# Kernel tuning notes

Measured on AMD Instinct MI355X. Metric: run time of the kernel, lower is better.

## Reference

```python
import jax, jax.numpy as jnp
import numpy as np

R = 32  # voxel resolution


def _swish(x):
    return x * jax.nn.sigmoid(x)


def _group_norm(x, gamma, beta, groups, eps=1e-5):
    B, C = x.shape[0], x.shape[1]
    xr = x.reshape(B, groups, -1)
    mean = xr.mean(-1, keepdims=True)
    var = xr.var(-1, keepdims=True)
    xn = ((xr - mean) * jax.lax.rsqrt(var + eps)).reshape(x.shape)
    bshape = (1, C) + (1,) * (x.ndim - 2)
    return xn * gamma.reshape(bshape) + beta.reshape(bshape)


def _conv3d_same(x, w, b):
    # x: [B,C,D,H,W], w: [O,I,k,k,k], SAME padding (k//2)
    k = w.shape[-1]
    p = k // 2
    y = jax.lax.conv_general_dilated(
        x, w, window_strides=(1, 1, 1), padding=[(p, p)] * 3,
        dimension_numbers=('NCDHW', 'OIDHW', 'NCDHW'))
    return y + b[None, :, None, None, None]


def setup_inputs() -> dict:
    key = jax.random.key(0)
    ks = jax.random.split(key, 8)
    B, Cin, Cout, N = 8, 64, 128, 16384
    return {
        'features': jax.random.normal(ks[0], (B, Cin, N), jnp.float32),
        'coords': jax.random.normal(ks[1], (B, 3, N), jnp.float32),
        'temb': jnp.zeros((1,), jnp.float32),
        'w1': jax.random.normal(ks[2], (Cout, Cin, 3, 3, 3), jnp.float32) * 0.02,
        'b1': jnp.zeros((Cout,), jnp.float32),
        'g1_gamma': jnp.ones((Cout,), jnp.float32),
        'g1_beta': jnp.zeros((Cout,), jnp.float32),
        'w2': jax.random.normal(ks[3], (Cout, Cout, 3, 3, 3), jnp.float32) * 0.02,
        'b2': jnp.zeros((Cout,), jnp.float32),
        'g2_gamma': jnp.ones((Cout,), jnp.float32),
        'g2_beta': jnp.zeros((Cout,), jnp.float32),
        'wp': jax.random.normal(ks[4], (Cout, Cin), jnp.float32) * 0.02,
        'bp': jnp.zeros((Cout,), jnp.float32),
        'gp_gamma': jnp.ones((Cout,), jnp.float32),
        'gp_beta': jnp.zeros((Cout,), jnp.float32),
    }


def reference(features, coords, temb, w1, b1, g1_gamma, g1_beta,
              w2, b2, g2_gamma, g2_beta, wp, bp, gp_gamma, gp_beta):
    B, Cin, N = features.shape
    Cout = w1.shape[0]

    # ---- Voxelization (coords are detached in original; no coord grads) ----
    coords_c = jax.lax.stop_gradient(coords)
    nc = coords_c - coords_c.mean(axis=2, keepdims=True)            # [B,3,N]
    nrm = jnp.linalg.norm(nc, axis=1, keepdims=True)                # [B,1,N]
    nc = nc / (nrm.max(axis=2, keepdims=True) * 2.0) + 0.5          # eps=0
    nc = jnp.clip(nc * R, 0.0, R - 1)                               # norm_coords
    vox_idx = jnp.clip(jnp.round(nc).astype(jnp.int32), 0, R - 1)   # [B,3,N]

    flat = (vox_idx[:, 0] * R + vox_idx[:, 1]) * R + vox_idx[:, 2]  # [B,N]
    seg = (flat + jnp.arange(B, dtype=flat.dtype)[:, None] * (R ** 3)).reshape(-1)
    feat_bn = features.transpose(0, 2, 1).reshape(B * N, Cin)       # [B*N,Cin]
    sums = jax.ops.segment_sum(feat_bn, seg, num_segments=B * R ** 3)
    cnts = jax.ops.segment_sum(jnp.ones((B * N,), features.dtype), seg,
                               num_segments=B * R ** 3)
    vox = sums / jnp.maximum(cnts, 1.0)[:, None]                    # avg voxelize
    vox = vox.reshape(B, R, R, R, Cin).transpose(0, 4, 1, 2, 3)     # [B,Cin,R,R,R]

    # ---- Voxel branch: conv3d -> GN -> Swish -> (dropout: eval, no-op) -> conv3d -> GN -> Swish ----
    vox = _swish(_group_norm(_conv3d_same(vox, w1, b1), g1_gamma, g1_beta, 8))
    vox = _swish(_group_norm(_conv3d_same(vox, w2, b2), g2_gamma, g2_beta, 8))

    # ---- Trilinear devoxelize ----
    c = jnp.clip(nc, 0.0, R - 1 - 1e-6)                             # [B,3,N]
    idx0f = jnp.floor(c)
    frac = c - idx0f
    i0 = idx0f.astype(jnp.int32)
    i1 = jnp.minimum(i0 + 1, R - 1)
    vox_flat = vox.reshape(B, Cout, R ** 3)

    def corner(ix, iy, iz):
        fl = (ix * R + iy) * R + iz                                 # [B,N]
        return jnp.take_along_axis(vox_flat, fl[:, None, :], axis=2)  # [B,Cout,N]

    x0, y0, z0 = i0[:, 0], i0[:, 1], i0[:, 2]
    x1, y1, z1 = i1[:, 0], i1[:, 1], i1[:, 2]
    dx = frac[:, 0][:, None, :]
    dy = frac[:, 1][:, None, :]
    dz = frac[:, 2][:, None, :]
    devox = (corner(x0, y0, z0) * (1 - dx) * (1 - dy) * (1 - dz)
             + corner(x0, y0, z1) * (1 - dx) * (1 - dy) * dz
             + corner(x0, y1, z0) * (1 - dx) * dy * (1 - dz)
             + corner(x0, y1, z1) * (1 - dx) * dy * dz
             + corner(x1, y0, z0) * dx * (1 - dy) * (1 - dz)
             + corner(x1, y0, z1) * dx * (1 - dy) * dz
             + corner(x1, y1, z0) * dx * dy * (1 - dz)
             + corner(x1, y1, z1) * dx * dy * dz)                   # [B,Cout,N]

    # ---- Point branch: 1x1 conv1d -> GN(8) -> Swish ----
    pf = jnp.einsum('oc,bcn->bon', wp, features) + bp[None, :, None]
    pf = _swish(_group_norm(pf, gp_gamma, gp_beta, 8))

    fused = devox + pf
    return fused
```

## Files before the change

kernel.cpp:

```cpp
#include <hip/hip_runtime.h>
#include <hip/hip_bf16.h>
#include <cmath>

#define BATCH 8
#define CIN 64
#define COUT 128
#define NPTS 16384
#define RES 32
#define R3 32768
#define NGROUP 8
#define GSIZE 16

typedef __hip_bfloat16 bf16;
typedef __attribute__((ext_vector_type(8))) short short8;
typedef __attribute__((ext_vector_type(4))) float f32x4;

__device__ inline float b2f(ushort u) { union { float f; uint v; } x; x.v = ((uint)u) << 16; return x.f; }
__device__ inline ushort f2bu(float f) { __hip_bfloat16 h = __float2bfloat16(f); return *reinterpret_cast<ushort*>(&h); }

__global__ __launch_bounds__(256) void coord_stats_k(const float* __restrict__ coords,
                                                     float* __restrict__ bstats) {
    int b = blockIdx.x;
    int t = threadIdx.x;
    __shared__ float red[256];
    __shared__ float means[3];
    for (int c = 0; c < 3; ++c) {
        float acc = 0.f;
        const float* p = coords + ((size_t)b * 3 + c) * NPTS;
        for (int n = t; n < NPTS; n += 256) acc += p[n];
        red[t] = acc; __syncthreads();
        for (int s = 128; s > 0; s >>= 1) { if (t < s) red[t] += red[t + s]; __syncthreads(); }
        if (t == 0) means[c] = red[0] * (1.f / NPTS);
        __syncthreads();
    }
    float m0 = means[0], m1 = means[1], m2 = means[2];
    const float* px = coords + ((size_t)b * 3 + 0) * NPTS;
    const float* py = coords + ((size_t)b * 3 + 1) * NPTS;
    const float* pz = coords + ((size_t)b * 3 + 2) * NPTS;
    float mx = 0.f;
    for (int n = t; n < NPTS; n += 256) {
        float dx = px[n] - m0, dy = py[n] - m1, dz = pz[n] - m2;
        mx = fmaxf(mx, sqrtf(dx * dx + dy * dy + dz * dz));
    }
    red[t] = mx; __syncthreads();
    for (int s = 128; s > 0; s >>= 1) { if (t < s) red[t] = fmaxf(red[t], red[t + s]); __syncthreads(); }
    if (t == 0) {
        bstats[b * 4 + 0] = m0; bstats[b * 4 + 1] = m1; bstats[b * 4 + 2] = m2;
        bstats[b * 4 + 3] = 1.f / (2.f * red[0]);
    }
}

__global__ __launch_bounds__(256) void vox_idx_k(const float* __restrict__ coords,
                                                 const float* __restrict__ bstats,
                                                 float4* __restrict__ nc4,
                                                 int* __restrict__ vidx,
                                                 int* __restrict__ slot,
                                                 unsigned int* __restrict__ cnts) {
    int g = blockIdx.x * 256 + threadIdx.x;
    int b = g >> 14, n = g & (NPTS - 1);
    float m0 = bstats[b * 4 + 0], m1 = bstats[b * 4 + 1], m2 = bstats[b * 4 + 2];
    float sc = bstats[b * 4 + 3];
    float x = coords[((size_t)b * 3 + 0) * NPTS + n];
    float y = coords[((size_t)b * 3 + 1) * NPTS + n];
    float z = coords[((size_t)b * 3 + 2) * NPTS + n];
    float ncx = fminf(fmaxf(((x - m0) * sc + 0.5f) * (float)RES, 0.f), RES - 1.f);
    float ncy = fminf(fmaxf(((y - m1) * sc + 0.5f) * (float)RES, 0.f), RES - 1.f);
    float ncz = fminf(fmaxf(((z - m2) * sc + 0.5f) * (float)RES, 0.f), RES - 1.f);
    nc4[g] = make_float4(ncx, ncy, ncz, 0.f);
    int ix = min(max((int)rintf(ncx), 0), RES - 1);
    int iy = min(max((int)rintf(ncy), 0), RES - 1);
    int iz = min(max((int)rintf(ncz), 0), RES - 1);
    int v = b * R3 + (ix * RES + iy) * RES + iz;
    vidx[g] = v;
    slot[g] = (int)atomicAdd(&cnts[v], 1u);
}

__global__ __launch_bounds__(256) void transpose_feats_k(const float* __restrict__ feats,
                                                         float* __restrict__ featT) {
    int blk = blockIdx.x;
    int b = blk >> 8, ntile = blk & 255;
    int t = threadIdx.x;
    __shared__ float lds[64][65];
    for (int e = t; e < 64 * 64; e += 256) {
        int c = e >> 6, n = e & 63;
        lds[c][n] = feats[((size_t)b * CIN + c) * NPTS + ntile * 64 + n];
    }
    __syncthreads();
    for (int e = t; e < 64 * 64; e += 256) {
        int n = e >> 6, c = e & 63;
        featT[(((size_t)b << 14) + ntile * 64 + n) * CIN + c] = lds[c][n];
    }
}

__global__ __launch_bounds__(256) void scan1_k(const unsigned int* __restrict__ cnts,
                                               unsigned int* __restrict__ offs,
                                               unsigned int* __restrict__ part) {
    int t = threadIdx.x;
    int g = blockIdx.x * 256 + t;
    unsigned int v = cnts[g];
    __shared__ unsigned int s[256];
    s[t] = v; __syncthreads();
    for (int d = 1; d < 256; d <<= 1) {
        unsigned int x = (t >= d) ? s[t - d] : 0u;
        __syncthreads();
        s[t] += x;
        __syncthreads();
    }
    offs[g] = s[t] - v;
    if (t == 255) part[blockIdx.x] = s[255];
}

__global__ __launch_bounds__(1024) void scan2_k(unsigned int* __restrict__ part) {
    int t = threadIdx.x;
    unsigned int v = part[t];
    __shared__ unsigned int s[1024];
    s[t] = v; __syncthreads();
    for (int d = 1; d < 1024; d <<= 1) {
        unsigned int x = (t >= d) ? s[t - d] : 0u;
        __syncthreads();
        s[t] += x;
        __syncthreads();
    }
    part[t] = s[t] - v;
}

__global__ __launch_bounds__(256) void scan3_k(unsigned int* __restrict__ offs,
                                               const unsigned int* __restrict__ part) {
    int g = blockIdx.x * 256 + threadIdx.x;
    offs[g] += part[blockIdx.x];
}

__global__ __launch_bounds__(256) void scatter_pts_k(const int* __restrict__ vidx,
                                                     const int* __restrict__ slot,
                                                     const unsigned int* __restrict__ offs,
                                                     unsigned int* __restrict__ pidx2) {
    int g = blockIdx.x * 256 + threadIdx.x;
    int v = vidx[g];
    pidx2[offs[v] + slot[g]] = (unsigned int)g;
}

__global__ __launch_bounds__(256) void gather_k(const float* __restrict__ featT,
                                                const unsigned int* __restrict__ cnts,
                                                const unsigned int* __restrict__ offs,
                                                const unsigned int* __restrict__ pidx2,
                                                bf16* __restrict__ voxCL) {
    int u = blockIdx.x * 256 + threadIdx.x;
    int v = u >> 3;
    int l8 = u & 7;
    unsigned int cnt = cnts[v];
    unsigned int off = offs[v];
    float acc[8] = {0.f, 0.f, 0.f, 0.f, 0.f, 0.f, 0.f, 0.f};
    for (unsigned int i = 0; i < cnt; ++i) {
        unsigned int g = pidx2[off + i];
        const float4* fp = (const float4*)(featT + (size_t)g * CIN + l8 * 8);
        float4 f0 = fp[0], f1 = fp[1];
        acc[0] += f0.x; acc[1] += f0.y; acc[2] += f0.z; acc[3] += f0.w;
        acc[4] += f1.x; acc[5] += f1.y; acc[6] += f1.z; acc[7] += f1.w;
    }
    float inv = 1.f / fmaxf((float)cnt, 1.f);
    ushort o[8];
#pragma unroll
    for (int j = 0; j < 8; ++j) o[j] = f2bu(acc[j] * inv);
    *(short8*)(voxCL + (size_t)v * CIN + l8 * 8) = *(short8*)o;
}

template <int CIN_T>
__global__ __launch_bounds__(256) void wreorder_k(const float* __restrict__ w,
                                                  bf16* __restrict__ wf) {
    const int NC = CIN_T / 32;
    int u = blockIdx.x * 256 + threadIdx.x;
    if (u >= 27 * NC * 128 * 4) return;
    int kb = u & 3;
    int co = (u >> 2) & 127;
    int c32 = (u >> 9) % NC;
    int t = u / (512 * NC);
    int cibase = c32 * 32 + kb * 8;
    ushort o[8];
#pragma unroll
    for (int j = 0; j < 8; ++j)
        o[j] = f2bu(w[((size_t)co * CIN_T + cibase + j) * 27 + t]);
    *(short8*)(wf + (size_t)u * 8) = *(short8*)o;
}

__global__ __launch_bounds__(256) void wpt_k(const float* __restrict__ wp,
                                             float* __restrict__ wpT) {
    int u = blockIdx.x * 256 + threadIdx.x;
    int co = u & 127, ci = u >> 7;
    wpT[ci * 128 + co] = wp[co * 64 + ci];
}

template <int CIN_T>
__global__ __launch_bounds__(512, 2) void conv3d_mfma_k(const bf16* __restrict__ x,
                                                        const bf16* __restrict__ wf,
                                                        const float* __restrict__ bias,
                                                        bf16* __restrict__ y,
                                                        float* __restrict__ gnacc) {
    constexpr int NC = CIN_T / 32;
    int blk = blockIdx.x;
    int hq = blk & 7;
    int d = (blk >> 3) & 31;
    int b = blk >> 8;
    int t = threadIdx.x;
    int lane = t & 63;
    int wid = t >> 6;
    int cog = wid >> 1;
    int sg = wid & 1;
    int lr = lane & 15;
    int kb = lane >> 4;

    __shared__ __align__(16) char xs[3 * 6 * 34 * 80];
    __shared__ float gred[8][2];
    if (t < 16) gred[t >> 1][t & 1] = 0.f;

    f32x4 acc[2][4];
#pragma unroll
    for (int r = 0; r < 2; ++r)
#pragma unroll
        for (int j = 0; j < 4; ++j) acc[r][j] = (f32x4){0.f, 0.f, 0.f, 0.f};

    int bbase[4];
#pragma unroll
    for (int j = 0; j < 4; ++j) {
        int sp = sg * 64 + j * 16 + lr;
        int hl = sp >> 5, wl = sp & 31;
        bbase[j] = (hl * 34 + wl) * 80 + kb * 16;
    }

    for (int cc = 0; cc < NC; ++cc) {
        __syncthreads();
        for (int e = t; e < 612 * 4; e += 512) {
            int ekb = e & 3;
            int pos = e >> 2;
            int ww = pos % 34;
            int hh = (pos / 34) % 6;
            int dd = pos / 204;
            int dz = d + dd - 1;
            int hz = hq * 4 + hh - 1;
            int wz = ww - 1;
            short8 v = {0, 0, 0, 0, 0, 0, 0, 0};
            if (dz >= 0 && dz < RES && hz >= 0 && hz < RES && wz >= 0 && wz < RES)
                v = *(const short8*)(x + ((size_t)b * R3 + dz * 1024 + hz * 32 + wz) * CIN_T + cc * 32 + ekb * 8);
            *(short8*)(xs + pos * 80 + ekb * 16) = v;
        }
        __syncthreads();

        const short8* wfp = (const short8*)wf;
        size_t abase = ((size_t)cc * 128 + cog * 32 + lr) * 4 + kb;
#pragma unroll
        for (int dd = 0; dd < 3; ++dd)
#pragma unroll
            for (int dh = 0; dh < 3; ++dh)
#pragma unroll
                for (int dw = 0; dw < 3; ++dw) {
                    int tap = (dd * 3 + dh) * 3 + dw;
                    short8 a0 = wfp[abase + (size_t)tap * NC * 512];
                    short8 a1 = wfp[abase + (size_t)tap * NC * 512 + 64];
                    int toff = ((dd * 6 + dh) * 34 + dw) * 80;
                    short8 bb[4];
#pragma unroll
                    for (int j = 0; j < 4; ++j)
                        bb[j] = *(const short8*)(xs + bbase[j] + toff);
#pragma unroll
                    for (int j = 0; j < 4; ++j) {
                        acc[0][j] = __builtin_amdgcn_mfma_f32_16x16x32_bf16(a0, bb[j], acc[0][j], 0, 0, 0);
                        acc[1][j] = __builtin_amdgcn_mfma_f32_16x16x32_bf16(a1, bb[j], acc[1][j], 0, 0, 0);
                    }
                }
    }

    float sred[2], ssred[2];
#pragma unroll
    for (int r = 0; r < 2; ++r) {
        int co = cog * 32 + r * 16 + kb * 4;
        float4 bv = *(const float4*)(bias + co);
        float s = 0.f, ss = 0.f;
#pragma unroll
        for (int j = 0; j < 4; ++j) {
            int sp = sg * 64 + j * 16 + lr;
            int p = d * 1024 + (hq * 4 + (sp >> 5)) * 32 + (sp & 31);
            float v0 = acc[r][j][0] + bv.x;
            float v1 = acc[r][j][1] + bv.y;
            float v2 = acc[r][j][2] + bv.z;
            float v3 = acc[r][j][3] + bv.w;
            ushort4 o;
            o.x = f2bu(v0); o.y = f2bu(v1); o.z = f2bu(v2); o.w = f2bu(v3);
            *(ushort4*)(y + ((size_t)b * R3 + p) * COUT + co) = o;
            s += v0 + v1 + v2 + v3;
            ss += v0 * v0 + v1 * v1 + v2 * v2 + v3 * v3;
        }
        sred[r] = s; ssred[r] = ss;
    }
#pragma unroll
    for (int m = 1; m < 64; m <<= 1) {
#pragma unroll
        for (int r = 0; r < 2; ++r) {
            sred[r] += __shfl_xor(sred[r], m, 64);
            ssred[r] += __shfl_xor(ssred[r], m, 64);
        }
    }
    if (lane == 0) {
#pragma unroll
        for (int r = 0; r < 2; ++r) {
            atomicAdd(&gred[cog * 2 + r][0], sred[r]);
            atomicAdd(&gred[cog * 2 + r][1], ssred[r]);
        }
    }
    __syncthreads();
    if (t < 16) atomicAdd(&gnacc[(b * 8 + (t >> 1)) * 2 + (t & 1)], gred[t >> 1][t & 1]);
}

__global__ __launch_bounds__(256) void gn_apply_cl_k(bf16* __restrict__ x,
                                                     const float* __restrict__ gnacc,
                                                     const float* __restrict__ gamma,
                                                     const float* __restrict__ beta) {
    int u = blockIdx.x * 256 + threadIdx.x;
    int ci8 = u & 15;
    int p = (u >> 4) & (R3 - 1);
    int b = u >> 19;
    int ci = ci8 * 8;
    int bg = b * 8 + (ci8 >> 1);
    const float M = (float)(GSIZE * R3);
    float s = gnacc[bg * 2], ss = gnacc[bg * 2 + 1];
    float mean = s / M;
    float istd = rsqrtf(fmaxf(ss / M - mean * mean, 0.f) + 1e-5f);
    bf16* ptr = x + ((size_t)b * R3 + p) * COUT + ci;
    short8 v = *(const short8*)ptr;
    ushort o[8];
#pragma unroll
    for (int j = 0; j < 8; ++j) {
        float f = b2f((ushort)v[j]);
        float yv = fmaf((f - mean) * istd, gamma[ci + j], beta[ci + j]);
        o[j] = f2bu(yv / (1.f + __expf(-yv)));
    }
    *(short8*)ptr = *(short8*)o;
}

__global__ __launch_bounds__(256) void pstats_cl_k(const float* __restrict__ featT,
                                                   const float* __restrict__ wpT,
                                                   const float* __restrict__ bp,
                                                   bf16* __restrict__ pfb,
                                                   float* __restrict__ gnacc) {
    __shared__ float wls[64 * 128];
    __shared__ float gred[8][2];
    int t = threadIdx.x;
    for (int e = t; e < 64 * 128 / 4; e += 256)
        ((float4*)wls)[e] = ((const float4*)wpT)[e];
    if (t < 16) gred[t >> 1][t & 1] = 0.f;
    __syncthreads();

    int u = blockIdx.x * 256 + t;
    int g = u >> 3;
    int l8 = u & 7;
    int b = g >> 14;
    int c0 = l8 * 16;

    float a[16];
#pragma unroll
    for (int k = 0; k < 16; ++k) a[k] = bp[c0 + k];
    const float* fg = featT + (size_t)g * CIN;
    for (int ci = 0; ci < CIN; ++ci) {
        float fv = fg[ci];
        const float* wrow = wls + ci * 128 + c0;
#pragma unroll
        for (int k = 0; k < 16; ++k) a[k] = fmaf(wrow[k], fv, a[k]);
    }
    ushort o_[16];
#pragma unroll
    for (int k = 0; k < 16; ++k) o_[k] = f2bu(a[k]);
    *(short8*)(pfb + (size_t)g * COUT + c0) = *(short8*)(o_);
    *(short8*)(pfb + (size_t)g * COUT + c0 + 8) = *(short8*)(o_ + 8);

    float s = 0.f, ss = 0.f;
#pragma unroll
    for (int k = 0; k < 16; ++k) { s += a[k]; ss = fmaf(a[k], a[k], ss); }
    s += __shfl_xor(s, 8, 64);  ss += __shfl_xor(ss, 8, 64);
    s += __shfl_xor(s, 16, 64); ss += __shfl_xor(ss, 16, 64);
    s += __shfl_xor(s, 32, 64); ss += __shfl_xor(ss, 32, 64);
    int lane = t & 63;
    if (lane < 8) {
        atomicAdd(&gred[lane][0], s);
        atomicAdd(&gred[lane][1], ss);
    }
    __syncthreads();
    if (t < 16) atomicAdd(&gnacc[(b * 8 + (t >> 1)) * 2 + (t & 1)], gred[t >> 1][t & 1]);
}

__global__ __launch_bounds__(256) void fuse2_k(const bf16* __restrict__ vox,
                                               const bf16* __restrict__ pfb,
                                               const float4* __restrict__ nc4,
                                               const unsigned int* __restrict__ pidx2,
                                               const float* __restrict__ gn2acc,
                                               const float* __restrict__ gnpacc,
                                               const float* __restrict__ g2g,
                                               const float* __restrict__ g2b,
                                               const float* __restrict__ gpg,
                                               const float* __restrict__ gpb,
                                               float* __restrict__ pfT) {
    int t = threadIdx.x;
    int u = blockIdx.x * 256 + t;
    int s = u >> 3;
    int l8 = u & 7;
    unsigned int g = pidx2[s];
    int b = (int)(g >> 14);
    int c0 = l8 * 16;

    const short8* pfp = (const short8*)(pfb + (size_t)g * COUT + c0);
    short8 p0 = pfp[0], p1 = pfp[1];
    float a[16];
#pragma unroll
    for (int j = 0; j < 8; ++j) { a[j] = b2f((ushort)p0[j]); a[8 + j] = b2f((ushort)p1[j]); }

    int bg = b * 8 + l8;
    const float M2 = (float)(GSIZE * R3);
    const float Mp = (float)(GSIZE * NPTS);
    float s2 = gn2acc[bg * 2], ss2 = gn2acc[bg * 2 + 1];
    float mean2 = s2 / M2;
    float istd2 = rsqrtf(fmaxf(ss2 / M2 - mean2 * mean2, 0.f) + 1e-5f);
    float sp = gnpacc[bg * 2], ssp = gnpacc[bg * 2 + 1];
    float meanp = sp / Mp;
    float istdp = rsqrtf(fmaxf(ssp / Mp - meanp * meanp, 0.f) + 1e-5f);
    float ga[16], gb[16];
#pragma unroll
    for (int j = 0; j < 16; ++j) {
        float gm = g2g[c0 + j];
        ga[j] = istd2 * gm;
        gb[j] = g2b[c0 + j] - mean2 * istd2 * gm;
    }

    float4 c4 = nc4[g];
    const float CMAX = (float)(RES - 1) - 1e-6f;
    float cx = fminf(c4.x, CMAX), cy = fminf(c4.y, CMAX), cz = fminf(c4.z, CMAX);
    int ix0 = (int)cx, iy0 = (int)cy, iz0 = (int)cz;
    float fx = cx - ix0, fy = cy - iy0, fz = cz - iz0;
    int ix1 = min(ix0 + 1, RES - 1), iy1 = min(iy0 + 1, RES - 1), iz1 = min(iz0 + 1, RES - 1);
    float gx0 = 1.f - fx, gy0 = 1.f - fy, gz0 = 1.f - fz;
    float wc[8] = {gx0 * gy0 * gz0, gx0 * gy0 * fz, gx0 * fy * gz0, gx0 * fy * fz,
                   fx * gy0 * gz0,  fx * gy0 * fz,  fx * fy * gz0,  fx * fy * fz};
    int fi[8];
    fi[0] = (ix0 * RES + iy0) * RES + iz0; fi[1] = (ix0 * RES + iy0) * RES + iz1;
    fi[2] = (ix0 * RES + iy1) * RES + iz0; fi[3] = (ix0 * RES + iy1) * RES + iz1;
    fi[4] = (ix1 * RES + iy0) * RES + iz0; fi[5] = (ix1 * RES + iy0) * RES + iz1;
    fi[6] = (ix1 * RES + iy1) * RES + iz0; fi[7] = (ix1 * RES + iy1) * RES + iz1;

    const bf16* vb = vox + (size_t)b * R3 * COUT + c0;
    float accv[16] = {0.f, 0.f, 0.f, 0.f, 0.f, 0.f, 0.f, 0.f,
                      0.f, 0.f, 0.f, 0.f, 0.f, 0.f, 0.f, 0.f};
#pragma unroll
    for (int f = 0; f < 8; ++f) {
        const short8* vp = (const short8*)(vb + (size_t)fi[f] * COUT);
        short8 v0 = vp[0], v1 = vp[1];
        float wgt = wc[f];
#pragma unroll
        for (int j = 0; j < 8; ++j) {
            float yv = fmaf(b2f((ushort)v0[j]), ga[j], gb[j]);
            accv[j] = fmaf(wgt, yv / (1.f + __expf(-yv)), accv[j]);
        }
#pragma unroll
        for (int j = 0; j < 8; ++j) {
            float yv = fmaf(b2f((ushort)v1[j]), ga[8 + j], gb[8 + j]);
            accv[8 + j] = fmaf(wgt, yv / (1.f + __expf(-yv)), accv[8 + j]);
        }
    }

    float outv[16];
#pragma unroll
    for (int j = 0; j < 16; ++j) {
        float pm = gpg[c0 + j];
        float yv = fmaf((a[j] - meanp) * istdp, pm, gpb[c0 + j]);
        outv[j] = yv / (1.f + __expf(-yv)) + accv[j];
    }
    float* pp = pfT + (size_t)g * COUT + c0;
#pragma unroll
    for (int k = 0; k < 4; ++k)
        *(float4*)(pp + k * 4) = make_float4(outv[k*4], outv[k*4+1], outv[k*4+2], outv[k*4+3]);
}

__global__ __launch_bounds__(256) void transpose_out_k(const float* __restrict__ pfT,
                                                       float* __restrict__ out) {
    int blk = blockIdx.x;
    int b = blk >> 8, nt = blk & 255;
    int t = threadIdx.x;
    int n0 = nt * 64;
    __shared__ float lds[64][129];
#pragma unroll
    for (int k = 0; k < 8; ++k) {
        int e = t + k * 256;
        int row = e >> 5, c4 = e & 31;
        float4 v = ((const float4*)pfT)[(((size_t)b << 14) + n0 + row) * 32 + c4];
        lds[row][c4 * 4 + 0] = v.x;
        lds[row][c4 * 4 + 1] = v.y;
        lds[row][c4 * 4 + 2] = v.z;
        lds[row][c4 * 4 + 3] = v.w;
    }
    __syncthreads();
#pragma unroll
    for (int k = 0; k < 32; ++k) {
        int e = t + k * 256;
        int c = e >> 6, n = e & 63;
        out[((size_t)b * COUT + c) * NPTS + n0 + n] = lds[n][c];
    }
}

extern "C" void kernel_launch(void* const* d_in, const int* in_sizes, int n_in,
                              void* d_out, int out_size, void* d_ws, size_t ws_size,
                              hipStream_t stream) {
    const float* features = (const float*)d_in[0];
    const float* coords   = (const float*)d_in[1];
    const float* w1  = (const float*)d_in[3];
    const float* b1  = (const float*)d_in[4];
    const float* g1g = (const float*)d_in[5];
    const float* g1b = (const float*)d_in[6];
    const float* w2  = (const float*)d_in[7];
    const float* b2  = (const float*)d_in[8];
    const float* g2g = (const float*)d_in[9];
    const float* g2b = (const float*)d_in[10];
    const float* wp  = (const float*)d_in[11];
    const float* bp  = (const float*)d_in[12];
    const float* gpg = (const float*)d_in[13];
    const float* gpb = (const float*)d_in[14];
    float* out = (float*)d_out;

    char* ws = (char*)d_ws;
    size_t off = 0;
    bf16* act1 = (bf16*)(ws + off);
    float* pfT = (float*)(ws + off);         off += (size_t)BATCH * R3 * COUT * 2;
    bf16* act2 = (bf16*)(ws + off);          off += (size_t)BATCH * R3 * COUT * 2;
    bf16* voxCL = (bf16*)(ws + off);
    bf16* pfb = (bf16*)(ws + off);           off += (size_t)BATCH * R3 * CIN * 2;
    float* featT = (float*)(ws + off);       off += (size_t)BATCH * NPTS * CIN * 4;
    bf16* w1f = (bf16*)(ws + off);           off += (size_t)27 * 2 * 128 * 32 * 2;
    bf16* w2f = (bf16*)(ws + off);           off += (size_t)27 * 4 * 128 * 32 * 2;
    float* wpT = (float*)(ws + off);         off += 64 * 128 * 4;
    float4* nc4 = (float4*)(ws + off);       off += (size_t)BATCH * NPTS * 16;
    unsigned int* cnts = (unsigned int*)(ws + off);  off += (size_t)BATCH * R3 * 4;
    unsigned int* offs = (unsigned int*)(ws + off);  off += (size_t)BATCH * R3 * 4;
    int* vidx = (int*)(ws + off);            off += (size_t)BATCH * NPTS * 4;
    int* slot = (int*)(ws + off);            off += (size_t)BATCH * NPTS * 4;
    unsigned int* pidx2 = (unsigned int*)(ws + off); off += (size_t)BATCH * NPTS * 4;
    unsigned int* part = (unsigned int*)(ws + off);  off += 4096;
    float* bstats = (float*)(ws + off);      off += 256;
    float* gn1acc = (float*)(ws + off);      off += 512;
    float* gn2acc = (float*)(ws + off);      off += 512;
    float* gnpacc = (float*)(ws + off);      off += 512;

    hipMemsetAsync(cnts, 0, (size_t)BATCH * R3 * 4, stream);
    hipMemsetAsync(gn1acc, 0, 3 * 512, stream);

    coord_stats_k<<<BATCH, 256, 0, stream>>>(coords, bstats);
    vox_idx_k<<<BATCH * NPTS / 256, 256, 0, stream>>>(coords, bstats, nc4, vidx, slot, cnts);
    transpose_feats_k<<<BATCH * 256, 256, 0, stream>>>(features, featT);
    scan1_k<<<BATCH * R3 / 256, 256, 0, stream>>>(cnts, offs, part);
    scan2_k<<<1, 1024, 0, stream>>>(part);
    scan3_k<<<BATCH * R3 / 256, 256, 0, stream>>>(offs, part);
    scatter_pts_k<<<BATCH * NPTS / 256, 256, 0, stream>>>(vidx, slot, offs, pidx2);
    gather_k<<<BATCH * R3 * 8 / 256, 256, 0, stream>>>(featT, cnts, offs, pidx2, voxCL);

    wreorder_k<CIN><<<(27 * 2 * 128 * 4 + 255) / 256, 256, 0, stream>>>(w1, w1f);
    wreorder_k<COUT><<<(27 * 4 * 128 * 4 + 255) / 256, 256, 0, stream>>>(w2, w2f);
    wpt_k<<<32, 256, 0, stream>>>(wp, wpT);

    conv3d_mfma_k<CIN><<<BATCH * 32 * 8, 512, 0, stream>>>(voxCL, w1f, b1, act1, gn1acc);
    gn_apply_cl_k<<<BATCH * R3 * 16 / 256, 256, 0, stream>>>(act1, gn1acc, g1g, g1b);

    conv3d_mfma_k<COUT><<<BATCH * 32 * 8, 512, 0, stream>>>(act1, w2f, b2, act2, gn2acc);

    pstats_cl_k<<<BATCH * NPTS * 8 / 256, 256, 0, stream>>>(featT, wpT, bp, pfb, gnpacc);

    fuse2_k<<<BATCH * NPTS * 8 / 256, 256, 0, stream>>>(act2, pfb, nc4, pidx2,
                                                        gn2acc, gnpacc, g2g, g2b, gpg, gpb, pfT);

    transpose_out_k<<<BATCH * 256, 256, 0, stream>>>(pfT, out);
}
```

Measured before the change: 693.7 us.

## Store transposed features in bf16 and run point conv1d on MFMA

The transposed feature buffer is now written in bf16 instead of fp32, which halves the bytes read by the voxel gather and by the point-branch GEMM. The scalar FMA point-branch 1x1 conv is replaced by an MFMA bf16 GEMM. A new kernel reorders the point weights into the MFMA fragment layout, and the group-norm statistics are reduced with wave shuffles. This adds bf16 rounding on input features before the voxel averaging and the point GEMM, which may cost some accuracy.

```diff
diff --git a/kernel.cpp b/kernel.cpp
--- a/kernel.cpp
+++ b/kernel.cpp
@@ -76,7 +76,7 @@
 }
 
 __global__ __launch_bounds__(256) void transpose_feats_k(const float* __restrict__ feats,
-                                                         float* __restrict__ featT) {
+                                                         bf16* __restrict__ featTb) {
     int blk = blockIdx.x;
     int b = blk >> 8, ntile = blk & 255;
     int t = threadIdx.x;
@@ -86,9 +86,12 @@
         lds[c][n] = feats[((size_t)b * CIN + c) * NPTS + ntile * 64 + n];
     }
     __syncthreads();
-    for (int e = t; e < 64 * 64; e += 256) {
-        int n = e >> 6, c = e & 63;
-        featT[(((size_t)b << 14) + ntile * 64 + n) * CIN + c] = lds[c][n];
+    for (int e = t; e < 64 * 8; e += 256) {
+        int n = e >> 3, oct = e & 7;
+        ushort o[8];
+#pragma unroll
+        for (int j = 0; j < 8; ++j) o[j] = f2bu(lds[oct * 8 + j][n]);
+        *(short8*)(featTb + ((((size_t)b << 14) + ntile * 64 + n) * CIN) + oct * 8) = *(short8*)o;
     }
 }
 
@@ -139,7 +142,7 @@
     pidx2[offs[v] + slot[g]] = (unsigned int)g;
 }
 
-__global__ __launch_bounds__(256) void gather_k(const float* __restrict__ featT,
+__global__ __launch_bounds__(256) void gather_k(const bf16* __restrict__ featTb,
                                                 const unsigned int* __restrict__ cnts,
                                                 const unsigned int* __restrict__ offs,
                                                 const unsigned int* __restrict__ pidx2,
@@ -152,10 +155,9 @@
     float acc[8] = {0.f, 0.f, 0.f, 0.f, 0.f, 0.f, 0.f, 0.f};
     for (unsigned int i = 0; i < cnt; ++i) {
         unsigned int g = pidx2[off + i];
-        const float4* fp = (const float4*)(featT + (size_t)g * CIN + l8 * 8);
-        float4 f0 = fp[0], f1 = fp[1];
-        acc[0] += f0.x; acc[1] += f0.y; acc[2] += f0.z; acc[3] += f0.w;
-        acc[4] += f1.x; acc[5] += f1.y; acc[6] += f1.z; acc[7] += f1.w;
+        short8 f = *(const short8*)(featTb + (size_t)g * CIN + l8 * 8);
+#pragma unroll
+        for (int j = 0; j < 8; ++j) acc[j] += b2f((ushort)f[j]);
     }
     float inv = 1.f / fmaxf((float)cnt, 1.f);
     ushort o[8];
@@ -182,11 +184,18 @@
     *(short8*)(wf + (size_t)u * 8) = *(short8*)o;
 }
 
-__global__ __launch_bounds__(256) void wpt_k(const float* __restrict__ wp,
-                                             float* __restrict__ wpT) {
+__global__ __launch_bounds__(256) void wpreorder_k(const float* __restrict__ wp,
+                                                   bf16* __restrict__ wpb) {
     int u = blockIdx.x * 256 + threadIdx.x;
-    int co = u & 127, ci = u >> 7;
-    wpT[ci * 128 + co] = wp[co * 64 + ci];
+    if (u >= 1024) return;
+    int kb = u & 3;
+    int co = (u >> 2) & 127;
+    int c32 = u >> 9;
+    ushort o[8];
+#pragma unroll
+    for (int j = 0; j < 8; ++j)
+        o[j] = f2bu(wp[(size_t)co * CIN + c32 * 32 + kb * 8 + j]);
+    *(short8*)(wpb + (size_t)u * 8) = *(short8*)o;
 }
 
 template <int CIN_T>
@@ -335,51 +344,78 @@
     *(short8*)ptr = *(short8*)o;
 }
 
-__global__ __launch_bounds__(256) void pstats_cl_k(const float* __restrict__ featT,
-                                                   const float* __restrict__ wpT,
-                                                   const float* __restrict__ bp,
-                                                   bf16* __restrict__ pfb,
-                                                   float* __restrict__ gnacc) {
-    __shared__ float wls[64 * 128];
+__global__ __launch_bounds__(256) void pgemm_mfma_k(const bf16* __restrict__ featTb,
+                                                    const bf16* __restrict__ wpb,
+                                                    const float* __restrict__ bp,
+                                                    bf16* __restrict__ pfb,
+                                                    float* __restrict__ gnacc) {
+    int t = threadIdx.x;
+    int lane = t & 63;
+    int cog = t >> 6;
+    int lr = lane & 15;
+    int kb = lane >> 4;
+    int g0 = blockIdx.x * 64;
+    int b = g0 >> 14;
+
     __shared__ float gred[8][2];
-    int t = threadIdx.x;
-    for (int e = t; e < 64 * 128 / 4; e += 256)
-        ((float4*)wls)[e] = ((const float4*)wpT)[e];
     if (t < 16) gred[t >> 1][t & 1] = 0.f;
-    __syncthreads();
-
-    int u = blockIdx.x * 256 + t;
-    int g = u >> 3;
-    int l8 = u & 7;
-    int b = g >> 14;
-    int c0 = l8 * 16;
-
-    float a[16];
-#pragma unroll
-    for (int k = 0; k < 16; ++k) a[k] = bp[c0 + k];
-    const float* fg = featT + (size_t)g * CIN;
-    for (int ci = 0; ci < CIN; ++ci) {
-        float fv = fg[ci];
-        const float* wrow = wls + ci * 128 + c0;
-#pragma unroll
-        for (int k = 0; k < 16; ++k) a[k] = fmaf(wrow[k], fv, a[k]);
-    }
-    ushort o_[16];
-#pragma unroll
-    for (int k = 0; k < 16; ++k) o_[k] = f2bu(a[k]);
-    *(short8*)(pfb + (size_t)g * COUT + c0) = *(short8*)(o_);
-    *(short8*)(pfb + (size_t)g * COUT + c0 + 8) = *(short8*)(o_ + 8);
-
-    float s = 0.f, ss = 0.f;
-#pragma unroll
-    for (int k = 0; k < 16; ++k) { s += a[k]; ss = fmaf(a[k], a[k], ss); }
-    s += __shfl_xor(s, 8, 64);  ss += __shfl_xor(ss, 8, 64);
-    s += __shfl_xor(s, 16, 64); ss += __shfl_xor(ss, 16, 64);
-    s += __shfl_xor(s, 32, 64); ss += __shfl_xor(ss, 32, 64);
-    int lane = t & 63;
-    if (lane < 8) {
-        atomicAdd(&gred[lane][0], s);
-        atomicAdd(&gred[lane][1], ss);
+
+    f32x4 acc[2][4];
+#pragma unroll
+    for (int r = 0; r < 2; ++r)
+#pragma unroll
+        for (int j = 0; j < 4; ++j) acc[r][j] = (f32x4){0.f, 0.f, 0.f, 0.f};
+
+    const short8* wfp = (const short8*)wpb;
+    const short8* ftp = (const short8*)featTb;
+#pragma unroll
+    for (int cc = 0; cc < 2; ++cc) {
+        size_t abase = ((size_t)cc * 128 + cog * 32 + lr) * 4 + kb;
+        short8 a0 = wfp[abase];
+        short8 a1 = wfp[abase + 64];
+#pragma unroll
+        for (int j = 0; j < 4; ++j) {
+            short8 bb = ftp[(size_t)(g0 + j * 16 + lr) * 8 + cc * 4 + kb];
+            acc[0][j] = __builtin_amdgcn_mfma_f32_16x16x32_bf16(a0, bb, acc[0][j], 0, 0, 0);
+            acc[1][j] = __builtin_amdgcn_mfma_f32_16x16x32_bf16(a1, bb, acc[1][j], 0, 0, 0);
+        }
+    }
+
+    float sred[2], ssred[2];
+#pragma unroll
+    for (int r = 0; r < 2; ++r) {
+        int co = cog * 32 + r * 16 + kb * 4;
+        float4 bv = *(const float4*)(bp + co);
+        float s = 0.f, ss = 0.f;
+#pragma unroll
+        for (int j = 0; j < 4; ++j) {
+            int g = g0 + j * 16 + lr;
+            float v0 = acc[r][j][0] + bv.x;
+            float v1 = acc[r][j][1] + bv.y;
+            float v2 = acc[r][j][2] + bv.z;
+            float v3 = acc[r][j][3] + bv.w;
+            ushort4 o;
+            o.x = f2bu(v0); o.y = f2bu(v1); o.z = f2bu(v2); o.w = f2bu(v3);
+            *(ushort4*)(pfb + (size_t)g * COUT + co) = o;
+            s += v0 + v1 + v2 + v3;
+            ss += v0 * v0 + v1 * v1 + v2 * v2 + v3 * v3;
+        }
+        sred[r] = s; ssred[r] = ss;
+    }
+#pragma unroll
+    for (int m = 1; m < 64; m <<= 1) {
+#pragma unroll
+        for (int r = 0; r < 2; ++r) {
+            sred[r] += __shfl_xor(sred[r], m, 64);
+            ssred[r] += __shfl_xor(ssred[r], m, 64);
+        }
+    }
+    if (lane == 0) {
+#pragma unroll
+        for (int r = 0; r < 2; ++r) {
+            atomicAdd(&gred[cog * 2 + r][0], sred[r]);
+            atomicAdd(&gred[cog * 2 + r][1], ssred[r]);
+        }
     }
     __syncthreads();
     if (t < 16) atomicAdd(&gnacc[(b * 8 + (t >> 1)) * 2 + (t & 1)], gred[t >> 1][t & 1]);
@@ -527,10 +563,10 @@
     bf16* act2 = (bf16*)(ws + off);          off += (size_t)BATCH * R3 * COUT * 2;
     bf16* voxCL = (bf16*)(ws + off);
     bf16* pfb = (bf16*)(ws + off);           off += (size_t)BATCH * R3 * CIN * 2;
-    float* featT = (float*)(ws + off);       off += (size_t)BATCH * NPTS * CIN * 4;
+    bf16* featTb = (bf16*)(ws + off);        off += (size_t)BATCH * NPTS * CIN * 2;
     bf16* w1f = (bf16*)(ws + off);           off += (size_t)27 * 2 * 128 * 32 * 2;
     bf16* w2f = (bf16*)(ws + off);           off += (size_t)27 * 4 * 128 * 32 * 2;
-    float* wpT = (float*)(ws + off);         off += 64 * 128 * 4;
+    bf16* wpb = (bf16*)(ws + off);           off += (size_t)2 * 128 * 32 * 2;
     float4* nc4 = (float4*)(ws + off);       off += (size_t)BATCH * NPTS * 16;
     unsigned int* cnts = (unsigned int*)(ws + off);  off += (size_t)BATCH * R3 * 4;
     unsigned int* offs = (unsigned int*)(ws + off);  off += (size_t)BATCH * R3 * 4;
@@ -548,23 +584,23 @@
 
     coord_stats_k<<<BATCH, 256, 0, stream>>>(coords, bstats);
     vox_idx_k<<<BATCH * NPTS / 256, 256, 0, stream>>>(coords, bstats, nc4, vidx, slot, cnts);
-    transpose_feats_k<<<BATCH * 256, 256, 0, stream>>>(features, featT);
+    transpose_feats_k<<<BATCH * 256, 256, 0, stream>>>(features, featTb);
     scan1_k<<<BATCH * R3 / 256, 256, 0, stream>>>(cnts, offs, part);
     scan2_k<<<1, 1024, 0, stream>>>(part);
     scan3_k<<<BATCH * R3 / 256, 256, 0, stream>>>(offs, part);
     scatter_pts_k<<<BATCH * NPTS / 256, 256, 0, stream>>>(vidx, slot, offs, pidx2);
-    gather_k<<<BATCH * R3 * 8 / 256, 256, 0, stream>>>(featT, cnts, offs, pidx2, voxCL);
+    gather_k<<<BATCH * R3 * 8 / 256, 256, 0, stream>>>(featTb, cnts, offs, pidx2, voxCL);
 
     wreorder_k<CIN><<<(27 * 2 * 128 * 4 + 255) / 256, 256, 0, stream>>>(w1, w1f);
     wreorder_k<COUT><<<(27 * 4 * 128 * 4 + 255) / 256, 256, 0, stream>>>(w2, w2f);
-    wpt_k<<<32, 256, 0, stream>>>(wp, wpT);
+    wpreorder_k<<<4, 256, 0, stream>>>(wp, wpb);
 
     conv3d_mfma_k<CIN><<<BATCH * 32 * 8, 512, 0, stream>>>(voxCL, w1f, b1, act1, gn1acc);
     gn_apply_cl_k<<<BATCH * R3 * 16 / 256, 256, 0, stream>>>(act1, gn1acc, g1g, g1b);
 
     conv3d_mfma_k<COUT><<<BATCH * 32 * 8, 512, 0, stream>>>(act1, w2f, b2, act2, gn2acc);
 
-    pstats_cl_k<<<BATCH * NPTS * 8 / 256, 256, 0, stream>>>(featT, wpT, bp, pfb, gnpacc);
+    pgemm_mfma_k<<<BATCH * NPTS / 64, 256, 0, stream>>>(featTb, wpb, bp, pfb, gnpacc);
 
     fuse2_k<<<BATCH * NPTS * 8 / 256, 256, 0, stream>>>(act2, pfb, nc4, pidx2,
                                                         gn2acc, gnpacc, g2g, g2b, gpg, gpb, pfT);
```

After: 644.2 us. 1.08x faster.
